# Optimization experiments

Measured on AMD Instinct MI355X. Metric: run time of the kernel, lower is better.

## Reference

```python
import jax, jax.numpy as jnp
import numpy as np

N = 100000      # nodes
E = 1600000     # random edges (self loops added in reference, like add_self_loops)
D_IN = 128
D_OUT = 128
NEG_SLOPE = 0.01  # F.leaky_relu default in the torch source


def setup_inputs() -> dict:
    key = jax.random.key(0)
    k_x, k_e, k_w, k_b, k_a, k_ab = jax.random.split(key, 6)
    x = jax.random.normal(k_x, (N, D_IN), dtype=jnp.float32)
    edge_index = jax.random.randint(k_e, (2, E), 0, N, dtype=jnp.int32)
    # small init scales keep exp(score) in a sane range (torch default init is also small)
    W_lin = jax.random.normal(k_w, (D_OUT, D_IN), dtype=jnp.float32) * 0.05
    b_lin = jax.random.normal(k_b, (D_OUT,), dtype=jnp.float32) * 0.05
    W_att = jax.random.normal(k_a, (1, 2 * D_OUT), dtype=jnp.float32) * 0.05
    b_att = jax.random.normal(k_ab, (1,), dtype=jnp.float32) * 0.05
    return {"x": x, "edge_index": edge_index, "W_lin": W_lin, "b_lin": b_lin,
            "W_att": W_att, "b_att": b_att}


def reference(x, edge_index, W_lin, b_lin, W_att, b_att):
    n = x.shape[0]
    d_out = W_lin.shape[0]
    # h = lin(x), computed ONCE (the torch loop redundantly recomputes it per edge)
    h = x @ W_lin.T + b_lin                      # [N, D_OUT]
    # add self loops (pyg_utils.add_self_loops)
    loops = jnp.arange(n, dtype=edge_index.dtype)
    src = jnp.concatenate([edge_index[0], loops])  # node i (attends over its out-neighbors)
    dst = jnp.concatenate([edge_index[1], loops])  # neighbor j
    # attention([h_i ; h_j]) = h_i . a_i + h_j . a_j + b
    a_i = W_att[0, :d_out]
    a_j = W_att[0, d_out:]
    score = h[src] @ a_i + h[dst] @ a_j + b_att[0]           # [E+N]
    score = jnp.where(score >= 0, score, NEG_SLOPE * score)  # leaky_relu(0.01)
    e = jnp.exp(score)                                        # plain exp, as in source (no max-shift)
    denom = jax.ops.segment_sum(e, src, num_segments=n)       # per-source softmax denominator
    alpha = e / denom[src]                                    # [E+N]
    msg = alpha[:, None] * h[dst]                             # [E+N, D_OUT]
    agg = jax.ops.segment_sum(msg, src, num_segments=n)       # attention_matrix @ h
    return jax.nn.elu(agg)
```

## Files before the change

### kernel.cpp

```cpp
#include <hip/hip_runtime.h>
#include <hip/hip_bf16.h>
#include <stdint.h>

typedef unsigned int uint;
typedef unsigned short ushort;

#define D 128
#define NEG_SLOPE 0.01f
#define BN 64
#define CAP 1280
#define NCHUNK 256
#define KMAX 2048

using frag_t = __attribute__((ext_vector_type(8))) short;
using f32x4  = __attribute__((ext_vector_type(4))) float;

__device__ __forceinline__ ushort f2bf(float f) {
    __hip_bfloat16 b = __float2bfloat16(f);
    ushort u; __builtin_memcpy(&u, &b, 2); return u;
}
__device__ __forceinline__ float bflo(uint p) { return __uint_as_float(p << 16); }
__device__ __forceinline__ float bfhi(uint p) { return __uint_as_float(p & 0xffff0000u); }

#define LDK 136

__global__ __launch_bounds__(256) void gemm_h(
    const float* __restrict__ x, const float* __restrict__ W,
    const float* __restrict__ bias, const float* __restrict__ Wa,
    const float* __restrict__ ba,
    ushort* __restrict__ h, float* __restrict__ si, float* __restrict__ sj, int n)
{
    __shared__ ushort xs[64 * LDK];
    __shared__ ushort wsh[128 * LDK];
    const int tid  = threadIdx.x;
    const int row0 = blockIdx.x * 64;

    {
        const int r = tid >> 5;
        const int k = (tid & 31) * 4;
#pragma unroll
        for (int i = 0; i < 8; ++i) {
            int lr = r + 8 * i;
            int gr = row0 + lr;
            int cr = gr < n ? gr : (n - 1);
            float4 v = *(const float4*)(x + (size_t)cr * D + k);
            ushort4 u; u.x = f2bf(v.x); u.y = f2bf(v.y); u.z = f2bf(v.z); u.w = f2bf(v.w);
            *(ushort4*)&xs[lr * LDK + k] = u;
        }
#pragma unroll
        for (int i = 0; i < 16; ++i) {
            int lr = r + 8 * i;
            float4 v = *(const float4*)(W + (size_t)lr * D + k);
            ushort4 u; u.x = f2bf(v.x); u.y = f2bf(v.y); u.z = f2bf(v.z); u.w = f2bf(v.w);
            *(ushort4*)&wsh[lr * LDK + k] = u;
        }
    }
    __syncthreads();

    const int wv   = tid >> 6;
    const int lane = tid & 63;
    const int mr   = lane & 15;
    const int qk   = (lane >> 4) * 8;

    f32x4 acc[8] = {};
    const ushort* xrow = xs + (16 * wv + mr) * LDK;
#pragma unroll
    for (int kk = 0; kk < 4; ++kk) {
        frag_t a = *(const frag_t*)(xrow + kk * 32 + qk);
#pragma unroll
        for (int t = 0; t < 8; ++t) {
            frag_t bf = *(const frag_t*)(wsh + (16 * t + mr) * LDK + kk * 32 + qk);
            acc[t] = __builtin_amdgcn_mfma_f32_16x16x32_bf16(a, bf, acc[t], 0, 0, 0);
        }
    }

    const int crow = 16 * wv + (lane >> 4) * 4;
    float pi[4] = {0.f, 0.f, 0.f, 0.f};
    float pj[4] = {0.f, 0.f, 0.f, 0.f};
#pragma unroll
    for (int t = 0; t < 8; ++t) {
        int col = 16 * t + mr;
        float bb = bias[col];
        float av = Wa[col];
        float bv = Wa[D + col];
#pragma unroll
        for (int r = 0; r < 4; ++r) {
            float v = acc[t][r] + bb;
            int grow = row0 + crow + r;
            if (grow < n) h[(size_t)grow * D + col] = f2bf(v);
            pi[r] += v * av;
            pj[r] += v * bv;
        }
    }
#pragma unroll
    for (int o = 1; o < 16; o <<= 1) {
#pragma unroll
        for (int r = 0; r < 4; ++r) {
            pi[r] += __shfl_xor(pi[r], o);
            pj[r] += __shfl_xor(pj[r], o);
        }
    }
    if (mr == 0) {
        float bav = ba[0];
#pragma unroll
        for (int r = 0; r < 4; ++r) {
            int grow = row0 + crow + r;
            if (grow < n) { si[grow] = pi[r] + bav; sj[grow] = pj[r]; }
        }
    }
}

__global__ __launch_bounds__(256) void count_k(
    const int* __restrict__ src, int* __restrict__ counts, int e, int K, int cpb)
{
    __shared__ int hist[KMAX];
    const int c = blockIdx.x;
    for (int i = threadIdx.x; i < K; i += 256) hist[i] = 0;
    __syncthreads();
    const int beg = c * cpb;
    const int end = min(e, beg + cpb);
    for (int i = beg + threadIdx.x; i < end; i += 256)
        atomicAdd(&hist[src[i] >> 6], 1);
    __syncthreads();
    for (int i = threadIdx.x; i < K; i += 256) counts[c * K + i] = hist[i];
}

__global__ __launch_bounds__(NCHUNK) void scan_chunks(
    int* __restrict__ counts, int* __restrict__ total, int K)
{
    __shared__ int s[NCHUNK];
    const int b = blockIdx.x, t = threadIdx.x;
    int v = counts[t * K + b];
    s[t] = v; __syncthreads();
#pragma unroll
    for (int o = 1; o < NCHUNK; o <<= 1) {
        int tv = (t >= o) ? s[t - o] : 0;
        __syncthreads();
        s[t] += tv;
        __syncthreads();
    }
    counts[t * K + b] = s[t] - v;
    if (t == NCHUNK - 1) total[b] = s[t];
}

__global__ __launch_bounds__(256) void fill_k(
    const int* __restrict__ src, const int* __restrict__ dst,
    const float* __restrict__ si, const float* __restrict__ sj,
    const int* __restrict__ cbase, uint2* __restrict__ barr,
    int e, int K, int cpb)
{
    __shared__ int cur[KMAX];
    const int c = blockIdx.x;
    for (int i = threadIdx.x; i < K; i += 256) cur[i] = cbase[c * K + i];
    __syncthreads();
    const int beg = c * cpb;
    const int end = min(e, beg + cpb);
    for (int i = beg + threadIdx.x; i < end; i += 256) {
        int s = src[i], d = dst[i];
        float sc = si[s] + sj[d];
        sc = sc >= 0.f ? sc : NEG_SLOPE * sc;
        float w = __expf(sc);
        int b = s >> 6;
        int p = atomicAdd(&cur[b], 1);
        if (p < CAP)
            barr[(size_t)b * CAP + p] =
                make_uint2(((uint)(s & (BN - 1)) << 17) | (uint)d, __float_as_uint(w));
    }
}

__global__ __launch_bounds__(512) void agg_k(
    const ushort* __restrict__ h, const uint2* __restrict__ barr,
    const int* __restrict__ total,
    const float* __restrict__ si, const float* __restrict__ sj,
    float* __restrict__ out, int n)
{
    __shared__ uint2 se[CAP];
    __shared__ int hist[BN];
    __shared__ int base[BN];
    __shared__ int cur[BN];
    const int b    = blockIdx.x;
    const int tid  = threadIdx.x;
    const int lane = tid & 63;
    const int wv   = tid >> 6;
    const int node0 = b << 6;

    if (tid < BN) hist[tid] = 0;
    __syncthreads();

    const int ecnt = min(total[b], CAP);
    const uint2* eb = barr + (size_t)b * CAP;

    uint2 r0 = make_uint2(0u, 0u), r1 = r0, r2 = r0;
    const bool v0 = tid < ecnt, v1 = tid + 512 < ecnt, v2 = tid + 1024 < ecnt;
    if (v0) { r0 = eb[tid];        atomicAdd(&hist[r0.x >> 17], 1); }
    if (v1) { r1 = eb[tid + 512];  atomicAdd(&hist[r1.x >> 17], 1); }
    if (v2) { r2 = eb[tid + 1024]; atomicAdd(&hist[r2.x >> 17], 1); }
    __syncthreads();

    if (tid < 64) {
        int v = hist[tid];
        int s = v;
#pragma unroll
        for (int o = 1; o < 64; o <<= 1) {
            int t = __shfl_up(s, o);
            if (lane >= o) s += t;
        }
        base[tid] = s - v;
        cur[tid]  = s - v;
    }
    __syncthreads();

    if (v0) se[atomicAdd(&cur[r0.x >> 17], 1)] = r0;
    if (v1) se[atomicAdd(&cur[r1.x >> 17], 1)] = r1;
    if (v2) se[atomicAdd(&cur[r2.x >> 17], 1)] = r2;
    __syncthreads();

    const uint lo = (uint)lane << 1;
#pragma unroll 1
    for (int t = 0; t < 8; ++t) {
        const int ls = (wv << 3) + t;
        const int node = node0 + ls;
        if (node >= n) break;

        float sc = si[node] + sj[node];
        sc = sc >= 0.f ? sc : NEG_SLOPE * sc;
        float w_ = __expf(sc);
        uint hv = *(const uint*)(h + (((uint)node << 7) + lo));
        float a0 = w_ * bflo(hv), a1 = w_ * bfhi(hv);
        float denom = w_;

        const int c = hist[ls];
        const uint2* seg = se + base[ls];
        int j = 0;
        for (; j + 4 <= c; j += 4) {
            uint2 w0 = seg[j], w1 = seg[j + 1], w2 = seg[j + 2], w3 = seg[j + 3];
            uint g0 = *(const uint*)(h + (((w0.x & 0x1FFFFu) << 7) + lo));
            uint g1 = *(const uint*)(h + (((w1.x & 0x1FFFFu) << 7) + lo));
            uint g2 = *(const uint*)(h + (((w2.x & 0x1FFFFu) << 7) + lo));
            uint g3 = *(const uint*)(h + (((w3.x & 0x1FFFFu) << 7) + lo));
            float e0 = __uint_as_float(w0.y), e1 = __uint_as_float(w1.y);
            float e2 = __uint_as_float(w2.y), e3 = __uint_as_float(w3.y);
            denom += (e0 + e1) + (e2 + e3);
            a0 += e0 * bflo(g0) + e1 * bflo(g1) + e2 * bflo(g2) + e3 * bflo(g3);
            a1 += e0 * bfhi(g0) + e1 * bfhi(g1) + e2 * bfhi(g2) + e3 * bfhi(g3);
        }
        for (; j < c; ++j) {
            uint2 w = seg[j];
            uint g = *(const uint*)(h + (((w.x & 0x1FFFFu) << 7) + lo));
            float we = __uint_as_float(w.y);
            denom += we;
            a0 += we * bflo(g);
            a1 += we * bfhi(g);
        }

        float inv = 1.f / denom;
        a0 *= inv; a1 *= inv;
        a0 = a0 > 0.f ? a0 : expm1f(a0);
        a1 = a1 > 0.f ? a1 : expm1f(a1);
        *(float2*)(out + (((uint)node << 7) + lo)) = make_float2(a0, a1);
    }
}

extern "C" void kernel_launch(void* const* d_in, const int* in_sizes, int n_in,
                              void* d_out, int out_size, void* d_ws, size_t ws_size,
                              hipStream_t stream)
{
    const float* x  = (const float*)d_in[0];
    const int*   ei = (const int*)  d_in[1];
    const float* Wl = (const float*)d_in[2];
    const float* bl = (const float*)d_in[3];
    const float* Wa = (const float*)d_in[4];
    const float* ba = (const float*)d_in[5];
    const int n = in_sizes[0] / D;
    const int e = in_sizes[1] / 2;
    const int* src = ei;
    const int* dst = ei + e;

    const int K   = (n + BN - 1) / BN;
    const int cpb = (e + NCHUNK - 1) / NCHUNK;

    char* w = (char*)d_ws;
    size_t off = 0;
    ushort* h      = (ushort*)(w + off); off += (size_t)n * D * 2;
    float*  si     = (float*) (w + off); off += (size_t)n * 4;
    float*  sj     = (float*) (w + off); off += (size_t)n * 4;
    int*    counts = (int*)   (w + off); off += (size_t)NCHUNK * K * 4;
    int*    total  = (int*)   (w + off); off += ((size_t)K * 4 + 15) & ~(size_t)15;
    uint2*  barr   = (uint2*) (w + off); off += (size_t)K * CAP * 8;

    gemm_h      <<<(n + 63) / 64, 256,    0, stream>>>(x, Wl, bl, Wa, ba, h, si, sj, n);
    count_k     <<<NCHUNK,        256,    0, stream>>>(src, counts, e, K, cpb);
    scan_chunks <<<K,             NCHUNK, 0, stream>>>(counts, total, K);
    fill_k      <<<NCHUNK,        256,    0, stream>>>(src, dst, si, sj, counts, barr, e, K, cpb);
    agg_k       <<<K,             512,    0, stream>>>(h, barr, total, si, sj, (float*)d_out, n);
}
```

Baseline: 260.6 us.

## Move edge weight computation into aggregation kernel and halve bucket entry size

Edge attention weights are no longer computed in the bucket-fill kernel. Bucket entries shrink from 8-byte (index, weight) pairs to 4-byte packed indices, and the aggregation kernel computes the weights after loading each bucket, with per-node si/sj cached in shared memory. The gather loop is also unrolled to 8 edges per iteration so more loads are in flight. This halves the bucket write and read traffic and removes random si/sj reads from fill, at the cost of random sj reads inside the aggregation kernel and more registers from the wider unroll.

```diff
diff --git a/kernel.cpp b/kernel.cpp
--- a/kernel.cpp
+++ b/kernel.cpp
@@ -145,8 +145,7 @@
 
 __global__ __launch_bounds__(256) void fill_k(
     const int* __restrict__ src, const int* __restrict__ dst,
-    const float* __restrict__ si, const float* __restrict__ sj,
-    const int* __restrict__ cbase, uint2* __restrict__ barr,
+    const int* __restrict__ cbase, uint* __restrict__ barr,
     int e, int K, int cpb)
 {
     __shared__ int cur[KMAX];
@@ -157,19 +156,15 @@
     const int end = min(e, beg + cpb);
     for (int i = beg + threadIdx.x; i < end; i += 256) {
         int s = src[i], d = dst[i];
-        float sc = si[s] + sj[d];
-        sc = sc >= 0.f ? sc : NEG_SLOPE * sc;
-        float w = __expf(sc);
         int b = s >> 6;
         int p = atomicAdd(&cur[b], 1);
         if (p < CAP)
-            barr[(size_t)b * CAP + p] =
-                make_uint2(((uint)(s & (BN - 1)) << 17) | (uint)d, __float_as_uint(w));
+            barr[(size_t)b * CAP + p] = ((uint)(s & (BN - 1)) << 17) | (uint)d;
     }
 }
 
 __global__ __launch_bounds__(512) void agg_k(
-    const ushort* __restrict__ h, const uint2* __restrict__ barr,
+    const ushort* __restrict__ h, const uint* __restrict__ barr,
     const int* __restrict__ total,
     const float* __restrict__ si, const float* __restrict__ sj,
     float* __restrict__ out, int n)
@@ -178,23 +173,49 @@
     __shared__ int hist[BN];
     __shared__ int base[BN];
     __shared__ int cur[BN];
+    __shared__ float si_s[BN];
+    __shared__ float sj_s[BN];
     const int b    = blockIdx.x;
     const int tid  = threadIdx.x;
     const int lane = tid & 63;
     const int wv   = tid >> 6;
     const int node0 = b << 6;
 
-    if (tid < BN) hist[tid] = 0;
+    if (tid < BN) {
+        hist[tid] = 0;
+        int nd = node0 + tid;
+        si_s[tid] = nd < n ? si[nd] : 0.f;
+        sj_s[tid] = nd < n ? sj[nd] : 0.f;
+    }
     __syncthreads();
 
     const int ecnt = min(total[b], CAP);
-    const uint2* eb = barr + (size_t)b * CAP;
-
-    uint2 r0 = make_uint2(0u, 0u), r1 = r0, r2 = r0;
+    const uint* eb = barr + (size_t)b * CAP;
+
+    uint p0 = 0, p1 = 0, p2 = 0;
+    float w0 = 0.f, w1 = 0.f, w2 = 0.f;
     const bool v0 = tid < ecnt, v1 = tid + 512 < ecnt, v2 = tid + 1024 < ecnt;
-    if (v0) { r0 = eb[tid];        atomicAdd(&hist[r0.x >> 17], 1); }
-    if (v1) { r1 = eb[tid + 512];  atomicAdd(&hist[r1.x >> 17], 1); }
-    if (v2) { r2 = eb[tid + 1024]; atomicAdd(&hist[r2.x >> 17], 1); }
+    if (v0) {
+        p0 = eb[tid];
+        float sc = si_s[p0 >> 17] + sj[p0 & 0x1FFFFu];
+        sc = sc >= 0.f ? sc : NEG_SLOPE * sc;
+        w0 = __expf(sc);
+        atomicAdd(&hist[p0 >> 17], 1);
+    }
+    if (v1) {
+        p1 = eb[tid + 512];
+        float sc = si_s[p1 >> 17] + sj[p1 & 0x1FFFFu];
+        sc = sc >= 0.f ? sc : NEG_SLOPE * sc;
+        w1 = __expf(sc);
+        atomicAdd(&hist[p1 >> 17], 1);
+    }
+    if (v2) {
+        p2 = eb[tid + 1024];
+        float sc = si_s[p2 >> 17] + sj[p2 & 0x1FFFFu];
+        sc = sc >= 0.f ? sc : NEG_SLOPE * sc;
+        w2 = __expf(sc);
+        atomicAdd(&hist[p2 >> 17], 1);
+    }
     __syncthreads();
 
     if (tid < 64) {
@@ -210,9 +231,9 @@
     }
     __syncthreads();
 
-    if (v0) se[atomicAdd(&cur[r0.x >> 17], 1)] = r0;
-    if (v1) se[atomicAdd(&cur[r1.x >> 17], 1)] = r1;
-    if (v2) se[atomicAdd(&cur[r2.x >> 17], 1)] = r2;
+    if (v0) se[atomicAdd(&cur[p0 >> 17], 1)] = make_uint2(p0, __float_as_uint(w0));
+    if (v1) se[atomicAdd(&cur[p1 >> 17], 1)] = make_uint2(p1, __float_as_uint(w1));
+    if (v2) se[atomicAdd(&cur[p2 >> 17], 1)] = make_uint2(p2, __float_as_uint(w2));
     __syncthreads();
 
     const uint lo = (uint)lane << 1;
@@ -222,7 +243,7 @@
         const int node = node0 + ls;
         if (node >= n) break;
 
-        float sc = si[node] + sj[node];
+        float sc = si_s[ls] + sj_s[ls];
         sc = sc >= 0.f ? sc : NEG_SLOPE * sc;
         float w_ = __expf(sc);
         uint hv = *(const uint*)(h + (((uint)node << 7) + lo));
@@ -232,17 +253,38 @@
         const int c = hist[ls];
         const uint2* seg = se + base[ls];
         int j = 0;
-        for (; j + 4 <= c; j += 4) {
-            uint2 w0 = seg[j], w1 = seg[j + 1], w2 = seg[j + 2], w3 = seg[j + 3];
-            uint g0 = *(const uint*)(h + (((w0.x & 0x1FFFFu) << 7) + lo));
-            uint g1 = *(const uint*)(h + (((w1.x & 0x1FFFFu) << 7) + lo));
-            uint g2 = *(const uint*)(h + (((w2.x & 0x1FFFFu) << 7) + lo));
-            uint g3 = *(const uint*)(h + (((w3.x & 0x1FFFFu) << 7) + lo));
-            float e0 = __uint_as_float(w0.y), e1 = __uint_as_float(w1.y);
-            float e2 = __uint_as_float(w2.y), e3 = __uint_as_float(w3.y);
-            denom += (e0 + e1) + (e2 + e3);
-            a0 += e0 * bflo(g0) + e1 * bflo(g1) + e2 * bflo(g2) + e3 * bflo(g3);
-            a1 += e0 * bfhi(g0) + e1 * bfhi(g1) + e2 * bfhi(g2) + e3 * bfhi(g3);
+        for (; j + 8 <= c; j += 8) {
+            uint2 ww[8];
+#pragma unroll
+            for (int i = 0; i < 8; ++i) ww[i] = seg[j + i];
+            uint gg[8];
+#pragma unroll
+            for (int i = 0; i < 8; ++i)
+                gg[i] = *(const uint*)(h + (((ww[i].x & 0x1FFFFu) << 7) + lo));
+#pragma unroll
+            for (int i = 0; i < 8; ++i) {
+                float ei = __uint_as_float(ww[i].y);
+                denom += ei;
+                a0 += ei * bflo(gg[i]);
+                a1 += ei * bfhi(gg[i]);
+            }
+        }
+        if (j + 4 <= c) {
+            uint2 ww[4];
+#pragma unroll
+            for (int i = 0; i < 4; ++i) ww[i] = seg[j + i];
+            uint gg[4];
+#pragma unroll
+            for (int i = 0; i < 4; ++i)
+                gg[i] = *(const uint*)(h + (((ww[i].x & 0x1FFFFu) << 7) + lo));
+#pragma unroll
+            for (int i = 0; i < 4; ++i) {
+                float ei = __uint_as_float(ww[i].y);
+                denom += ei;
+                a0 += ei * bflo(gg[i]);
+                a1 += ei * bfhi(gg[i]);
+            }
+            j += 4;
         }
         for (; j < c; ++j) {
             uint2 w = seg[j];
@@ -286,11 +328,11 @@
     float*  sj     = (float*) (w + off); off += (size_t)n * 4;
     int*    counts = (int*)   (w + off); off += (size_t)NCHUNK * K * 4;
     int*    total  = (int*)   (w + off); off += ((size_t)K * 4 + 15) & ~(size_t)15;
-    uint2*  barr   = (uint2*) (w + off); off += (size_t)K * CAP * 8;
+    uint*   barr   = (uint*)  (w + off); off += (size_t)K * CAP * 4;
 
     gemm_h      <<<(n + 63) / 64, 256,    0, stream>>>(x, Wl, bl, Wa, ba, h, si, sj, n);
     count_k     <<<NCHUNK,        256,    0, stream>>>(src, counts, e, K, cpb);
     scan_chunks <<<K,             NCHUNK, 0, stream>>>(counts, total, K);
-    fill_k      <<<NCHUNK,        256,    0, stream>>>(src, dst, si, sj, counts, barr, e, K, cpb);
+    fill_k      <<<NCHUNK,        256,    0, stream>>>(src, dst, counts, barr, e, K, cpb);
     agg_k       <<<K,             512,    0, stream>>>(h, barr, total, si, sj, (float*)d_out, n);
 }
```

After: 249.3 us. 1.05x faster.
